# Optimization experiments

Hardware: AMD Instinct MI355X
Metric: run time of the kernel (lower is better)

Reference implementation:

```python
import jax, jax.numpy as jnp
import numpy as np

S, B, D, H, DFF = 1024, 8, 1024, 16, 4096
HD = D // H
EPS = 1e-5


def layernorm(x, g, b):
    m = jnp.mean(x, axis=-1, keepdims=True)
    v = jnp.mean(jnp.square(x - m), axis=-1, keepdims=True)
    return (x - m) * jax.lax.rsqrt(v + EPS) * g + b


def setup_inputs() -> dict:
    key = jax.random.key(0)
    ks = jax.random.split(key, 6)
    w = 0.02
    return {
        "src": jax.random.normal(ks[0], (S, B, D), dtype=jnp.float32),
        "in_proj_w": jax.random.normal(ks[1], (3 * D, D), dtype=jnp.float32) * w,
        "in_proj_b": jnp.zeros((3 * D,), dtype=jnp.float32),
        "out_w": jax.random.normal(ks[2], (D, D), dtype=jnp.float32) * w,
        "out_b": jnp.zeros((D,), dtype=jnp.float32),
        "lin1_w": jax.random.normal(ks[3], (DFF, D), dtype=jnp.float32) * w,
        "lin1_b": jnp.zeros((DFF,), dtype=jnp.float32),
        "lin2_w": jax.random.normal(ks[4], (D, DFF), dtype=jnp.float32) * w,
        "lin2_b": jnp.zeros((D,), dtype=jnp.float32),
        "n1_g": jnp.ones((D,), dtype=jnp.float32),
        "n1_b": jnp.zeros((D,), dtype=jnp.float32),
        "n2_g": jnp.ones((D,), dtype=jnp.float32),
        "n2_b": jnp.zeros((D,), dtype=jnp.float32),
    }


def reference(src, in_proj_w, in_proj_b, out_w, out_b,
              lin1_w, lin1_b, lin2_w, lin2_b,
              n1_g, n1_b, n2_g, n2_b):
    # self-attention block (eval mode: dropout = identity)
    qkv = jnp.einsum('sbd,ed->sbe', src, in_proj_w) + in_proj_b  # [S,B,3D]
    q, k, v = jnp.split(qkv, 3, axis=-1)
    q = q.reshape(S, B, H, HD) * (1.0 / np.sqrt(HD)).astype(np.float32)
    k = k.reshape(S, B, H, HD)
    v = v.reshape(S, B, H, HD)
    scores = jnp.einsum('sbhd,tbhd->bhst', q, k)        # [B,H,S,S]
    attn = jax.nn.softmax(scores, axis=-1)
    o = jnp.einsum('bhst,tbhd->sbhd', attn, v).reshape(S, B, D)
    o = jnp.einsum('sbd,ed->sbe', o, out_w) + out_b
    # post-LN residuals
    x = layernorm(src + o, n1_g, n1_b)
    h = jax.nn.relu(jnp.einsum('sbd,fd->sbf', x, lin1_w) + lin1_b)
    f = jnp.einsum('sbf,df->sbd', h, lin2_w) + lin2_b
    return layernorm(x + f, n2_g, n2_b)
```

## Files before the change

### kernel.cpp

```cpp
#include <hip/hip_runtime.h>
#include <cstdint>
#include <cstddef>

#define S_  1024
#define B_  8
#define D_  1024
#define H_  16
#define HD_ 64
#define DFF_ 4096
#define M_  (S_*B_)
#define QKV_N (3*D_)

typedef float f32x4 __attribute__((ext_vector_type(4)));
typedef __bf16 bf16x8 __attribute__((ext_vector_type(8)));
typedef __bf16 bf16x4 __attribute__((ext_vector_type(4)));

#define GLDS16(gp, lp) __builtin_amdgcn_global_load_lds( \
    (__attribute__((address_space(1))) void*)(gp), \
    (__attribute__((address_space(3))) void*)(lp), 16, 0, 0)

#define CB0 (M_*D_/4)
#define CB1 (CB0 + QKV_N*D_/4)
#define CB2 (CB1 + D_*D_/4)
#define CB3 (CB2 + DFF_*D_/4)
#define CB4 (CB3 + D_*DFF_/4)

__global__ __launch_bounds__(256)
void cvt_all(const float* __restrict__ src, const float* __restrict__ w1f,
             const float* __restrict__ w2f, const float* __restrict__ w3f,
             const float* __restrict__ w4f,
             __bf16* __restrict__ src_bf, __bf16* __restrict__ w1,
             __bf16* __restrict__ w2, __bf16* __restrict__ w3,
             __bf16* __restrict__ w4)
{
    int i = blockIdx.x * 256 + threadIdx.x;
    const float* in; __bf16* out; int off;
    if      (i < CB0) { in = src; out = src_bf; off = 0;   }
    else if (i < CB1) { in = w1f; out = w1;     off = CB0; }
    else if (i < CB2) { in = w2f; out = w2;     off = CB1; }
    else if (i < CB3) { in = w3f; out = w3;     off = CB2; }
    else if (i < CB4) { in = w4f; out = w4;     off = CB3; }
    else return;
    int j = i - off;
    float4 v = *(const float4*)(in + (size_t)j * 4);
    __bf16 t[4] = {(__bf16)v.x, (__bf16)v.y, (__bf16)v.z, (__bf16)v.w};
    *(uint2*)(out + (size_t)j * 4) = *(uint2*)t;
}

template<bool OUT_BF16, bool RELU, bool ADD_BIAS, bool SPLITZ>
__global__ __launch_bounds__(256)
void gemm_bt(const __bf16* __restrict__ A, const __bf16* __restrict__ W,
             const float* __restrict__ bias,
             void* __restrict__ Cv0, void* __restrict__ Cv1,
             int M, int N, int Kloop, int lda)
{
    __shared__ __bf16 As[128 * 64];
    __shared__ __bf16 Bs[128 * 64];

    const int tid  = threadIdx.x;
    const int lane = tid & 63;
    const int wv   = tid >> 6;
    const int quad = lane >> 4;
    const int l15  = lane & 15;
    const int m0 = blockIdx.x * 128;
    const int n0 = blockIdx.y * 128;
    const int wm = (wv >> 1) * 64;
    const int wn = (wv & 1) * 64;

    void* Cv = Cv0;
    if (SPLITZ) {
        const int koff = blockIdx.z * Kloop;
        A += koff;
        W += koff;
        if (blockIdx.z) Cv = Cv1;
    }

    f32x4 acc[4][4] = {};

    for (int k0 = 0; k0 < Kloop; k0 += 64) {
        __syncthreads();
        #pragma unroll
        for (int j = 0; j < 4; ++j) {
            int c   = j * 256 + tid;
            int p   = c >> 9;
            int c2  = c & 511;
            int row = c2 >> 2;
            int cc  = c2 & 3;
            GLDS16(A + (size_t)(m0 + row) * lda + k0 + p * 32 + cc * 8,
                   (char*)As + p * 8192 + c2 * 16);
            GLDS16(W + (size_t)(n0 + row) * lda + k0 + p * 32 + cc * 8,
                   (char*)Bs + p * 8192 + c2 * 16);
        }
        __syncthreads();

        #pragma unroll
        for (int p = 0; p < 2; ++p) {
            bf16x8 af[4], bf[4];
            #pragma unroll
            for (int i = 0; i < 4; ++i)
                af[i] = *(const bf16x8*)(As + p * 4096 + (wm + i * 16 + l15) * 32 + quad * 8);
            #pragma unroll
            for (int j = 0; j < 4; ++j)
                bf[j] = *(const bf16x8*)(Bs + p * 4096 + (wn + j * 16 + l15) * 32 + quad * 8);
            #pragma unroll
            for (int i = 0; i < 4; ++i)
                #pragma unroll
                for (int j = 0; j < 4; ++j)
                    acc[i][j] = __builtin_amdgcn_mfma_f32_16x16x32_bf16(af[i], bf[j], acc[i][j], 0, 0, 0);
        }
    }

    #pragma unroll
    for (int j = 0; j < 4; ++j) {
        const int col = n0 + wn + j * 16 + l15;
        const float bv = ADD_BIAS ? bias[col] : 0.f;
        #pragma unroll
        for (int i = 0; i < 4; ++i) {
            const int rbase = m0 + wm + i * 16 + quad * 4;
            #pragma unroll
            for (int r = 0; r < 4; ++r) {
                float v = acc[i][j][r] + bv;
                if (RELU) v = fmaxf(v, 0.f);
                if (OUT_BF16)
                    ((__bf16*)Cv)[(size_t)(rbase + r) * N + col] = (__bf16)v;
                else
                    ((float*)Cv)[(size_t)(rbase + r) * N + col] = v;
            }
        }
    }
}

__global__ __launch_bounds__(256)
void v_transpose(const __bf16* __restrict__ qkv, __bf16* __restrict__ vt)
{
    __shared__ __bf16 T[64 * 65];
    const int tid = threadIdx.x;
    const int t0  = blockIdx.x * 64;
    const int bh  = blockIdx.y;
    const int b   = bh & (B_ - 1);
    const int h   = bh / B_;

    #pragma unroll
    for (int j = 0; j < 2; ++j) {
        int c = j * 256 + tid;
        int i = c >> 3, cc = c & 7;
        const __bf16* g = qkv + (size_t)((t0 + i) * B_ + b) * QKV_N + 2 * D_ + h * HD_ + cc * 8;
        bf16x8 v = *(const bf16x8*)g;
        #pragma unroll
        for (int u = 0; u < 8; ++u) T[(cc * 8 + u) * 65 + i] = v[u];
    }
    __syncthreads();
    #pragma unroll
    for (int j = 0; j < 2; ++j) {
        int c = j * 256 + tid;
        int d = c >> 3, cc = c & 7;
        __bf16 pk[8];
        #pragma unroll
        for (int u = 0; u < 8; ++u) pk[u] = T[d * 65 + cc * 8 + u];
        *(uint4*)(vt + ((size_t)bh * HD_ + d) * S_ + t0 + cc * 8) = *(uint4*)pk;
    }
}

#define TST 72

__global__ __launch_bounds__(256)
void attn_flash(const __bf16* __restrict__ qkv, const __bf16* __restrict__ vt,
                __bf16* __restrict__ out)
{
    __shared__ __bf16 Qs[64 * TST];
    __shared__ __bf16 Ks[64 * TST];
    __shared__ __bf16 Vt[64 * TST];
    __shared__ __bf16 Ps[64 * TST];

    const int tid  = threadIdx.x;
    const int lane = tid & 63;
    const int wv   = tid >> 6;
    const int quad = lane >> 4;
    const int l15  = lane & 15;
    const int s0 = blockIdx.x * 64;
    const int bh = blockIdx.y;
    const int b  = bh & (B_ - 1);
    const int h  = bh / B_;

    #pragma unroll
    for (int j = 0; j < 2; ++j) {
        int c = j * 256 + tid;
        int i = c >> 3, cc = c & 7;
        const __bf16* g = qkv + (size_t)((s0 + i) * B_ + b) * QKV_N + h * HD_ + cc * 8;
        *(uint4*)(Qs + i * TST + cc * 8) = *(const uint4*)g;
    }

    f32x4 oacc[4] = {};
    float m_run = -1e30f, l_run = 0.f;
    const float C2    = 0.125f * 1.44269504f;
    const float LOG2E = 1.44269504f;

    for (int t0 = 0; t0 < S_; t0 += 64) {
        __syncthreads();
        #pragma unroll
        for (int j = 0; j < 2; ++j) {
            int c = j * 256 + tid;
            int i = c >> 3, cc = c & 7;
            const __bf16* g = qkv + (size_t)((t0 + i) * B_ + b) * QKV_N + D_ + h * HD_ + cc * 8;
            *(uint4*)(Ks + i * TST + cc * 8) = *(const uint4*)g;
        }
        #pragma unroll
        for (int j = 0; j < 2; ++j) {
            int c = j * 256 + tid;
            int d = c >> 3, cc = c & 7;
            const __bf16* g = vt + ((size_t)bh * HD_ + d) * S_ + t0 + cc * 8;
            *(uint4*)(Vt + d * TST + cc * 8) = *(const uint4*)g;
        }
        __syncthreads();

        f32x4 sacc[4] = {};
        #pragma unroll
        for (int kk = 0; kk < 2; ++kk) {
            bf16x8 bq = *(const bf16x8*)(Qs + (wv * 16 + l15) * TST + kk * 32 + quad * 8);
            #pragma unroll
            for (int j = 0; j < 4; ++j) {
                bf16x8 ak = *(const bf16x8*)(Ks + (j * 16 + l15) * TST + kk * 32 + quad * 8);
                sacc[j] = __builtin_amdgcn_mfma_f32_16x16x32_bf16(ak, bq, sacc[j], 0, 0, 0);
            }
        }

        float mx = sacc[0][0];
        #pragma unroll
        for (int j = 0; j < 4; ++j)
            #pragma unroll
            for (int r = 0; r < 4; ++r) mx = fmaxf(mx, sacc[j][r]);
        mx = fmaxf(mx, __shfl_xor(mx, 16, 64));
        mx = fmaxf(mx, __shfl_xor(mx, 32, 64));
        float mnew = fmaxf(m_run, mx * 0.125f);
        float k1 = mnew * LOG2E;
        float rs = 0.f;
        #pragma unroll
        for (int j = 0; j < 4; ++j)
            #pragma unroll
            for (int r = 0; r < 4; ++r) {
                float p = __builtin_amdgcn_exp2f(sacc[j][r] * C2 - k1);
                sacc[j][r] = p;
                rs += p;
            }
        rs += __shfl_xor(rs, 16, 64);
        rs += __shfl_xor(rs, 32, 64);
        float alpha = __builtin_amdgcn_exp2f((m_run - mnew) * LOG2E);
        l_run = l_run * alpha + rs;
        m_run = mnew;

        #pragma unroll
        for (int j = 0; j < 4; ++j) {
            __bf16 pk[4] = {(__bf16)sacc[j][0], (__bf16)sacc[j][1],
                            (__bf16)sacc[j][2], (__bf16)sacc[j][3]};
            *(uint2*)(Ps + (wv * 16 + l15) * TST + j * 16 + quad * 4) = *(uint2*)pk;
        }

        #pragma unroll
        for (int r = 0; r < 4; ++r) {
            float ar = __shfl(alpha, quad * 4 + r, 64);
            #pragma unroll
            for (int jd = 0; jd < 4; ++jd) oacc[jd][r] *= ar;
        }

        #pragma unroll
        for (int kk = 0; kk < 2; ++kk) {
            bf16x8 ap = *(const bf16x8*)(Ps + (wv * 16 + l15) * TST + kk * 32 + quad * 8);
            #pragma unroll
            for (int jd = 0; jd < 4; ++jd) {
                bf16x8 bv = *(const bf16x8*)(Vt + (jd * 16 + l15) * TST + kk * 32 + quad * 8);
                oacc[jd] = __builtin_amdgcn_mfma_f32_16x16x32_bf16(ap, bv, oacc[jd], 0, 0, 0);
            }
        }
    }

    float linv = 1.f / l_run;
    #pragma unroll
    for (int r = 0; r < 4; ++r) {
        float lr = __shfl(linv, quad * 4 + r, 64);
        int s = s0 + wv * 16 + quad * 4 + r;
        #pragma unroll
        for (int jd = 0; jd < 4; ++jd) {
            int d = jd * 16 + l15;
            out[(size_t)(s * B_ + b) * D_ + h * HD_ + d] = (__bf16)(oacc[jd][r] * lr);
        }
    }
}

__global__ __launch_bounds__(256)
void ln_res3(const float* __restrict__ xa, const __bf16* __restrict__ p0,
             const __bf16* __restrict__ p1, const float* __restrict__ bias,
             const float* __restrict__ g, const float* __restrict__ beta,
             float* __restrict__ yout, __bf16* __restrict__ ybf)
{
    __shared__ float red[8];
    const int row = blockIdx.x;
    const int tid = threadIdx.x;
    const size_t base = (size_t)row * D_ + tid * 4;

    float4 a  = *(const float4*)(xa + base);
    bf16x4 q0 = *(const bf16x4*)(p0 + base);
    bf16x4 q1 = *(const bf16x4*)(p1 + base);
    float4 bb = *(const float4*)(bias + tid * 4);
    float x0 = a.x + (float)q0[0] + (float)q1[0] + bb.x;
    float x1 = a.y + (float)q0[1] + (float)q1[1] + bb.y;
    float x2 = a.z + (float)q0[2] + (float)q1[2] + bb.z;
    float x3 = a.w + (float)q0[3] + (float)q1[3] + bb.w;

    float s  = x0 + x1 + x2 + x3;
    float ss = x0 * x0 + x1 * x1 + x2 * x2 + x3 * x3;
    for (int msk = 1; msk <= 32; msk <<= 1) {
        s  += __shfl_xor(s,  msk, 64);
        ss += __shfl_xor(ss, msk, 64);
    }
    const int wv = tid >> 6;
    if ((tid & 63) == 0) { red[wv] = s; red[4 + wv] = ss; }
    __syncthreads();
    s  = red[0] + red[1] + red[2] + red[3];
    ss = red[4] + red[5] + red[6] + red[7];
    float mean = s * (1.f / D_);
    float var  = ss * (1.f / D_) - mean * mean;
    float rstd = rsqrtf(var + 1e-5f);

    float4 gv = *(const float4*)(g + tid * 4);
    float4 bv = *(const float4*)(beta + tid * 4);
    float y0 = (x0 - mean) * rstd * gv.x + bv.x;
    float y1 = (x1 - mean) * rstd * gv.y + bv.y;
    float y2 = (x2 - mean) * rstd * gv.z + bv.z;
    float y3 = (x3 - mean) * rstd * gv.w + bv.w;
    *(float4*)(yout + base) = make_float4(y0, y1, y2, y3);
    if (ybf) {
        __bf16 t[4] = {(__bf16)y0, (__bf16)y1, (__bf16)y2, (__bf16)y3};
        *(uint2*)(ybf + base) = *(uint2*)t;
    }
}

extern "C" void kernel_launch(void* const* d_in, const int* in_sizes, int n_in,
                              void* d_out, int out_size, void* d_ws, size_t ws_size,
                              hipStream_t stream)
{
    const float* src       = (const float*)d_in[0];
    const float* in_proj_w = (const float*)d_in[1];
    const float* in_proj_b = (const float*)d_in[2];
    const float* out_w     = (const float*)d_in[3];
    const float* out_b     = (const float*)d_in[4];
    const float* lin1_w    = (const float*)d_in[5];
    const float* lin1_b    = (const float*)d_in[6];
    const float* lin2_w    = (const float*)d_in[7];
    const float* lin2_b    = (const float*)d_in[8];
    const float* n1_g = (const float*)d_in[9];
    const float* n1_b = (const float*)d_in[10];
    const float* n2_g = (const float*)d_in[11];
    const float* n2_b = (const float*)d_in[12];

    char* ws = (char*)d_ws;
    size_t off = 0;
    auto alloc = [&](size_t bytes) { char* p = ws + off; off += (bytes + 255) & ~(size_t)255; return p; };

    __bf16* src_bf = (__bf16*)alloc((size_t)M_ * D_ * 2);
    __bf16* w1     = (__bf16*)alloc((size_t)QKV_N * D_ * 2);
    __bf16* w2     = (__bf16*)alloc((size_t)D_ * D_ * 2);
    __bf16* w3     = (__bf16*)alloc((size_t)DFF_ * D_ * 2);
    __bf16* w4     = (__bf16*)alloc((size_t)D_ * DFF_ * 2);
    __bf16* qkv    = (__bf16*)alloc((size_t)M_ * QKV_N * 2);
    char*   h_r    = alloc((size_t)M_ * DFF_ * 2);
    __bf16* xbf    = (__bf16*)alloc((size_t)M_ * D_ * 2);
    float*  xf     = (float*)alloc((size_t)M_ * D_ * 4);
    __bf16* vt     = (__bf16*)alloc((size_t)B_ * H_ * HD_ * S_ * 2);

    const size_t PART = (size_t)M_ * D_;
    __bf16* attn_o = src_bf;
    __bf16* o0 = (__bf16*)h_r;
    __bf16* o1 = o0 + PART;
    __bf16* hbf = (__bf16*)h_r;
    __bf16* f0 = vt;
    __bf16* f1 = xbf;

    cvt_all<<<(CB4 + 255) / 256, 256, 0, stream>>>(
        src, in_proj_w, out_w, lin1_w, lin2_w, src_bf, w1, w2, w3, w4);

    gemm_bt<true, false, true, false><<<dim3(M_ / 128, QKV_N / 128), 256, 0, stream>>>(
        src_bf, w1, in_proj_b, qkv, nullptr, M_, QKV_N, D_, D_);

    v_transpose<<<dim3(S_ / 64, B_ * H_), 256, 0, stream>>>(qkv, vt);

    attn_flash<<<dim3(S_ / 64, B_ * H_), 256, 0, stream>>>(qkv, vt, attn_o);

    gemm_bt<true, false, false, true><<<dim3(M_ / 128, D_ / 128, 2), 256, 0, stream>>>(
        attn_o, w2, nullptr, o0, o1, M_, D_, D_ / 2, D_);

    ln_res3<<<M_, 256, 0, stream>>>(src, o0, o1, out_b, n1_g, n1_b, xf, xbf);

    gemm_bt<true, true, true, false><<<dim3(M_ / 128, DFF_ / 128), 256, 0, stream>>>(
        xbf, w3, lin1_b, hbf, nullptr, M_, DFF_, D_, D_);

    gemm_bt<true, false, false, true><<<dim3(M_ / 128, D_ / 128, 2), 256, 0, stream>>>(
        hbf, w4, nullptr, f0, f1, M_, D_, DFF_ / 2, DFF_);

    ln_res3<<<M_, 256, 0, stream>>>(xf, f0, f1, lin2_b, n2_g, n2_b, (float*)d_out, nullptr);
}
```

Baseline: 538.3 us.

## Rewrite GEMMs with 256x256 tiles, triple-buffered LDS pipeline and grid swizzle

```diff
diff --git a/kernel.cpp b/kernel.cpp
--- a/kernel.cpp
+++ b/kernel.cpp
@@ -48,24 +48,30 @@
 }
 
 template<bool OUT_BF16, bool RELU, bool ADD_BIAS, bool SPLITZ>
-__global__ __launch_bounds__(256)
-void gemm_bt(const __bf16* __restrict__ A, const __bf16* __restrict__ W,
+__global__ __launch_bounds__(512, 2)
+void gemm256(const __bf16* __restrict__ A, const __bf16* __restrict__ W,
              const float* __restrict__ bias,
              void* __restrict__ Cv0, void* __restrict__ Cv1,
-             int M, int N, int Kloop, int lda)
-{
-    __shared__ __bf16 As[128 * 64];
-    __shared__ __bf16 Bs[128 * 64];
+             int N, int Kloop, int lda)
+{
+    extern __shared__ __bf16 lds[];
+    __bf16* As = lds;
+    __bf16* Bs = lds + 3 * 8192;
 
     const int tid  = threadIdx.x;
     const int lane = tid & 63;
     const int wv   = tid >> 6;
     const int quad = lane >> 4;
     const int l15  = lane & 15;
-    const int m0 = blockIdx.x * 128;
-    const int n0 = blockIdx.y * 128;
-    const int wm = (wv >> 1) * 64;
-    const int wn = (wv & 1) * 64;
+    const int wm   = (wv >> 2) * 128;
+    const int wn   = (wv & 3) * 64;
+
+    int id  = blockIdx.y * gridDim.x + blockIdx.x;
+    int nwg = gridDim.x * gridDim.y;
+    int q8  = nwg >> 3;
+    int swz = (id & 7) * q8 + (id >> 3);
+    const int m0 = (swz % gridDim.x) * 256;
+    const int n0 = (swz / gridDim.x) * 256;
 
     void* Cv = Cv0;
     if (SPLITZ) {
@@ -75,47 +81,66 @@
         if (blockIdx.z) Cv = Cv1;
     }
 
-    f32x4 acc[4][4] = {};
-
-    for (int k0 = 0; k0 < Kloop; k0 += 64) {
-        __syncthreads();
-        #pragma unroll
-        for (int j = 0; j < 4; ++j) {
-            int c   = j * 256 + tid;
-            int p   = c >> 9;
-            int c2  = c & 511;
-            int row = c2 >> 2;
-            int cc  = c2 & 3;
-            GLDS16(A + (size_t)(m0 + row) * lda + k0 + p * 32 + cc * 8,
-                   (char*)As + p * 8192 + c2 * 16);
-            GLDS16(W + (size_t)(n0 + row) * lda + k0 + p * 32 + cc * 8,
-                   (char*)Bs + p * 8192 + c2 * 16);
-        }
-        __syncthreads();
-
-        #pragma unroll
-        for (int p = 0; p < 2; ++p) {
-            bf16x8 af[4], bf[4];
-            #pragma unroll
-            for (int i = 0; i < 4; ++i)
-                af[i] = *(const bf16x8*)(As + p * 4096 + (wm + i * 16 + l15) * 32 + quad * 8);
+    const int nt = Kloop >> 5;
+
+    #define STAGE(kt, buf) do { \
+        const int k0s = (kt) << 5; \
+        _Pragma("unroll") \
+        for (int u = 0; u < 2; ++u) { \
+            int c = u * 512 + tid; \
+            int row = c >> 2, sl = c & 3; \
+            GLDS16(A + (size_t)(m0 + row) * lda + k0s + sl * 8, \
+                   (char*)(As + (buf) * 8192) + c * 16); \
+            GLDS16(W + (size_t)(n0 + row) * lda + k0s + sl * 8, \
+                   (char*)(Bs + (buf) * 8192) + c * 16); \
+        } \
+    } while (0)
+
+    STAGE(0, 0);
+    STAGE(1, 1);
+    asm volatile("s_waitcnt vmcnt(4)" ::: "memory");
+    __builtin_amdgcn_s_barrier();
+    __builtin_amdgcn_sched_barrier(0);
+
+    f32x4 acc[8][4] = {};
+
+    int cur = 0, stg = 2;
+    for (int t = 0; t < nt; ++t) {
+        if (t + 2 < nt) STAGE(t + 2, stg);
+
+        bf16x8 bf[4], af[8];
+        #pragma unroll
+        for (int j = 0; j < 4; ++j)
+            bf[j] = *(const bf16x8*)(Bs + cur * 8192 + (wn + j * 16 + l15) * 32 + quad * 8);
+        #pragma unroll
+        for (int i = 0; i < 8; ++i)
+            af[i] = *(const bf16x8*)(As + cur * 8192 + (wm + i * 16 + l15) * 32 + quad * 8);
+
+        __builtin_amdgcn_s_setprio(1);
+        #pragma unroll
+        for (int i = 0; i < 8; ++i)
             #pragma unroll
             for (int j = 0; j < 4; ++j)
-                bf[j] = *(const bf16x8*)(Bs + p * 4096 + (wn + j * 16 + l15) * 32 + quad * 8);
-            #pragma unroll
-            for (int i = 0; i < 4; ++i)
-                #pragma unroll
-                for (int j = 0; j < 4; ++j)
-                    acc[i][j] = __builtin_amdgcn_mfma_f32_16x16x32_bf16(af[i], bf[j], acc[i][j], 0, 0, 0);
-        }
-    }
+                acc[i][j] = __builtin_amdgcn_mfma_f32_16x16x32_bf16(af[i], bf[j], acc[i][j], 0, 0, 0);
+        __builtin_amdgcn_s_setprio(0);
+
+        if (t + 1 < nt) {
+            if (t + 2 < nt) { asm volatile("s_waitcnt vmcnt(4)" ::: "memory"); }
+            else            { asm volatile("s_waitcnt vmcnt(0)" ::: "memory"); }
+            __builtin_amdgcn_s_barrier();
+            __builtin_amdgcn_sched_barrier(0);
+        }
+        if (++cur == 3) cur = 0;
+        if (++stg == 3) stg = 0;
+    }
+    #undef STAGE
 
     #pragma unroll
     for (int j = 0; j < 4; ++j) {
         const int col = n0 + wn + j * 16 + l15;
         const float bv = ADD_BIAS ? bias[col] : 0.f;
         #pragma unroll
-        for (int i = 0; i < 4; ++i) {
+        for (int i = 0; i < 8; ++i) {
             const int rbase = m0 + wm + i * 16 + quad * 4;
             #pragma unroll
             for (int r = 0; r < 4; ++r) {
@@ -375,26 +400,28 @@
     __bf16* f0 = vt;
     __bf16* f1 = xbf;
 
+    const size_t SHM = 3 * 2 * 8192 * sizeof(__bf16);
+
     cvt_all<<<(CB4 + 255) / 256, 256, 0, stream>>>(
         src, in_proj_w, out_w, lin1_w, lin2_w, src_bf, w1, w2, w3, w4);
 
-    gemm_bt<true, false, true, false><<<dim3(M_ / 128, QKV_N / 128), 256, 0, stream>>>(
-        src_bf, w1, in_proj_b, qkv, nullptr, M_, QKV_N, D_, D_);
+    gemm256<true, false, true, false><<<dim3(M_ / 256, QKV_N / 256), 512, SHM, stream>>>(
+        src_bf, w1, in_proj_b, qkv, nullptr, QKV_N, D_, D_);
 
     v_transpose<<<dim3(S_ / 64, B_ * H_), 256, 0, stream>>>(qkv, vt);
 
     attn_flash<<<dim3(S_ / 64, B_ * H_), 256, 0, stream>>>(qkv, vt, attn_o);
 
-    gemm_bt<true, false, false, true><<<dim3(M_ / 128, D_ / 128, 2), 256, 0, stream>>>(
-        attn_o, w2, nullptr, o0, o1, M_, D_, D_ / 2, D_);
+    gemm256<true, false, false, true><<<dim3(M_ / 256, D_ / 256, 2), 512, SHM, stream>>>(
+        attn_o, w2, nullptr, o0, o1, D_, D_ / 2, D_);
 
     ln_res3<<<M_, 256, 0, stream>>>(src, o0, o1, out_b, n1_g, n1_b, xf, xbf);
 
-    gemm_bt<true, true, true, false><<<dim3(M_ / 128, DFF_ / 128), 256, 0, stream>>>(
-        xbf, w3, lin1_b, hbf, nullptr, M_, DFF_, D_, D_);
-
-    gemm_bt<true, false, false, true><<<dim3(M_ / 128, D_ / 128, 2), 256, 0, stream>>>(
-        hbf, w4, nullptr, f0, f1, M_, D_, DFF_ / 2, DFF_);
+    gemm256<true, true, true, false><<<dim3(M_ / 256, DFF_ / 256), 512, SHM, stream>>>(
+        xbf, w3, lin1_b, hbf, nullptr, DFF_, D_, D_);
+
+    gemm256<true, false, false, true><<<dim3(M_ / 256, D_ / 256, 2), 512, SHM, stream>>>(
+        hbf, w4, nullptr, f0, f1, D_, DFF_ / 2, DFF_);
 
     ln_res3<<<M_, 256, 0, stream>>>(xf, f0, f1, lin2_b, n2_g, n2_b, (float*)d_out, nullptr);
 }
```

Result: no change. 529.7 us (-1.6%).
